# Kernel tuning notes

Hardware: AMD Instinct MI355X
Metric: run time of the kernel (lower is better)

The kernel has to match this reference:

```python
import jax, jax.numpy as jnp
import numpy as np

C_Z = 128
C_H = 128
L = 512
EPS = 1e-5


def _layer_norm(x, w, b):
    mu = jnp.mean(x, axis=-1, keepdims=True)
    var = jnp.mean(jnp.square(x - mu), axis=-1, keepdims=True)
    return (x - mu) * jax.lax.rsqrt(var + EPS) * w + b


def setup_inputs() -> dict:
    key = jax.random.key(0)
    ks = jax.random.split(key, 10)
    s_z = 1.0 / np.sqrt(C_Z)
    s_h = 1.0 / np.sqrt(C_H)
    return {
        "z": jax.random.normal(ks[0], (L, L, C_Z), dtype=jnp.float32),
        "pair_mask": jax.random.randint(ks[1], (L, L), 0, 2, dtype=jnp.int32),
        "ln_in_w": jnp.ones((C_Z,), jnp.float32),
        "ln_in_b": jnp.zeros((C_Z,), jnp.float32),
        "ln_out_w": jnp.ones((C_H,), jnp.float32),
        "ln_out_b": jnp.zeros((C_H,), jnp.float32),
        # weights stored [in, out] so forward is x @ W
        "W_proj_a": jax.random.uniform(ks[2], (C_Z, C_H), jnp.float32, -s_z, s_z),
        "W_gate_a": jax.random.uniform(ks[3], (C_Z, C_H), jnp.float32, -s_z, s_z),
        "W_proj_b": jax.random.uniform(ks[4], (C_Z, C_H), jnp.float32, -s_z, s_z),
        "W_gate_b": jax.random.uniform(ks[5], (C_Z, C_H), jnp.float32, -s_z, s_z),
        "W_gate_out": jax.random.uniform(ks[6], (C_Z, C_Z), jnp.float32, -s_z, s_z),
        "W_proj_out": jax.random.uniform(ks[7], (C_H, C_Z), jnp.float32, -s_h, s_h),
    }


def reference(z, pair_mask, ln_in_w, ln_in_b, ln_out_w, ln_out_b,
              W_proj_a, W_gate_a, W_proj_b, W_gate_b, W_gate_out, W_proj_out):
    mask = pair_mask.astype(z.dtype)[..., None]  # [L, L, 1]
    z_ln = _layer_norm(z, ln_in_w, ln_in_b)      # [L, L, c_z]
    a = jax.nn.sigmoid(z_ln @ W_gate_a) * (z_ln @ W_proj_a) * mask  # [L, L, c_h]
    b = jax.nn.sigmoid(z_ln @ W_gate_b) * (z_ln @ W_proj_b) * mask  # [L, L, c_h]
    m = jnp.einsum('ikc,jkc->ijc', a, b)         # channel-batched matmul
    m_ln = _layer_norm(m, ln_out_w, ln_out_b)
    g = jax.nn.sigmoid(z_ln @ W_gate_out)        # [L, L, c_z]
    dz = g * (m_ln @ W_proj_out)
    return dz * mask
```

## Files before the change

kernel.cpp:

```cpp
#include <hip/hip_runtime.h>
#include <stdint.h>

#define LDIM 512
#define LLTOT 262144
#define EPSV 1e-5f

typedef short bf16x8 __attribute__((ext_vector_type(8)));
typedef float f32x4 __attribute__((ext_vector_type(4)));
typedef __attribute__((address_space(1))) unsigned as1_u32;
typedef __attribute__((address_space(3))) unsigned as3_u32;

__device__ __forceinline__ void stage16(const void* g, void* l) {
  __builtin_amdgcn_global_load_lds((as1_u32*)g, (as3_u32*)l, 16, 0, 0);
}

__device__ __forceinline__ unsigned short f2bf(float f) {
  union { float f; unsigned u; } v; v.f = f;
  unsigned r = v.u + 0x7FFFu + ((v.u >> 16) & 1u);
  return (unsigned short)(r >> 16);
}
__device__ __forceinline__ float bf2f(unsigned short h) {
  union { unsigned u; float f; } v; v.u = ((unsigned)h) << 16;
  return v.f;
}
__device__ __forceinline__ unsigned cvtpk(float lo, float hi) {
  unsigned r;
  asm("v_cvt_pk_bf16_f32 %0, %1, %2" : "=v"(r) : "v"(lo), "v"(hi));
  return r;
}
__device__ __forceinline__ float exp2h(float x) {
#if __has_builtin(__builtin_amdgcn_exp2f)
  return __builtin_amdgcn_exp2f(x);
#else
  float r; asm("v_exp_f32 %0, %1" : "=v"(r) : "v"(x)); return r;
#endif
}
__device__ __forceinline__ float rcph(float x) {
#if __has_builtin(__builtin_amdgcn_rcpf)
  return __builtin_amdgcn_rcpf(x);
#else
  float r; asm("v_rcp_f32 %0, %1" : "=v"(r) : "v"(x)); return r;
#endif
}
__device__ __forceinline__ float sigm(float x) {
  return rcph(1.0f + exp2h(x * -1.44269504f));
}


__global__ void k_prep(const float* __restrict__ Wpa, const float* __restrict__ Wga,
                       const float* __restrict__ Wpb, const float* __restrict__ Wgb,
                       const float* __restrict__ Wgo, const float* __restrict__ Wpo,
                       unsigned short* __restrict__ Wt) {
  int t = blockIdx.x * blockDim.x + threadIdx.x;
  int mat = t >> 14;
  int rem = t & 16383;
  int o = rem >> 7;
  int c = rem & 127;
  const float* src;
  switch (mat) {
    case 0: src = Wga; break;
    case 1: src = Wpa; break;
    case 2: src = Wgb; break;
    case 3: src = Wpb; break;
    case 4: src = Wgo; break;
    default: src = Wpo; break;
  }
  Wt[mat * 16384 + o * 128 + c] = f2bf(src[c * 128 + o]);
}

__global__ __launch_bounds__(256, 4) void k_proj(const float* __restrict__ z,
                                                 const float* __restrict__ lnw,
                                                 const float* __restrict__ lnb,
                                                 const unsigned short* __restrict__ Wt,
                                                 const int* __restrict__ maskp,
                                                 unsigned short* __restrict__ a_f,
                                                 unsigned short* __restrict__ b_f,
                                                 unsigned short* __restrict__ gout) {
  __shared__ __align__(16) unsigned char zbuf[128 * 272];
  __shared__ float maskf[128];
  const int t = threadIdx.x;
  const int bid = blockIdx.x;
  const long r0 = (long)bid * 128;
  const int w = t >> 6, lane = t & 63;
  const int mn = lane & 15, q4 = lane >> 4;
  const int k0 = (bid & 3) * 128;
  const long ibase = (long)(bid >> 2) * 131072;

  if (t < 128) maskf[t] = (float)maskp[r0 + t];

  {
    const int sub = lane >> 4, c16 = lane & 15;
    const float4 lw0 = ((const float4*)lnw)[c16 * 2];
    const float4 lw1 = ((const float4*)lnw)[c16 * 2 + 1];
    const float4 lb0 = ((const float4*)lnb)[c16 * 2];
    const float4 lb1 = ((const float4*)lnb)[c16 * 2 + 1];
#pragma unroll 2
    for (int rr = 0; rr < 8; ++rr) {
      const int row = w * 32 + rr * 4 + sub;
      const float4* zr = (const float4*)(z + (r0 + row) * 128);
      float4 v0 = zr[c16 * 2], v1 = zr[c16 * 2 + 1];
      float s = ((v0.x + v0.y) + (v0.z + v0.w)) + ((v1.x + v1.y) + (v1.z + v1.w));
      float q = v0.x * v0.x + v0.y * v0.y + v0.z * v0.z + v0.w * v0.w +
                v1.x * v1.x + v1.y * v1.y + v1.z * v1.z + v1.w * v1.w;
#pragma unroll
      for (int off = 8; off; off >>= 1) { s += __shfl_xor(s, off); q += __shfl_xor(q, off); }
      float mu = s * (1.0f / 128.0f);
      float rs = rsqrtf(q * (1.0f / 128.0f) - mu * mu + EPSV);
      uint4 o;
      o.x = cvtpk((v0.x - mu) * rs * lw0.x + lb0.x, (v0.y - mu) * rs * lw0.y + lb0.y);
      o.y = cvtpk((v0.z - mu) * rs * lw0.z + lb0.z, (v0.w - mu) * rs * lw0.w + lb0.w);
      o.z = cvtpk((v1.x - mu) * rs * lw1.x + lb1.x, (v1.y - mu) * rs * lw1.y + lb1.y);
      o.w = cvtpk((v1.z - mu) * rs * lw1.z + lb1.z, (v1.w - mu) * rs * lw1.w + lb1.w);
      *(uint4*)(&zbuf[row * 272 + c16 * 16]) = o;
    }
  }
  __syncthreads();

#pragma unroll 1
  for (int p = 0; p < 2; ++p) {
    const unsigned short* Wg = Wt + (p * 2) * 16384;
    const unsigned short* Wp = Wt + (p * 2 + 1) * 16384;
    unsigned short* dst = p ? b_f : a_f;
    bf16x8 wg[2][4], wp[2][4];
#pragma unroll
    for (int ntl = 0; ntl < 2; ++ntl)
#pragma unroll
      for (int kk = 0; kk < 4; ++kk) {
        const int o = (w * 2 + ntl) * 16 + mn;
        wg[ntl][kk] = *(const bf16x8*)(Wg + o * 128 + kk * 32 + q4 * 8);
        wp[ntl][kk] = *(const bf16x8*)(Wp + o * 128 + kk * 32 + q4 * 8);
      }
#pragma unroll 2
    for (int rg = 0; rg < 8; ++rg) {
      bf16x8 afr[4];
#pragma unroll
      for (int kk = 0; kk < 4; ++kk)
        afr[kk] = *(const bf16x8*)(&zbuf[(rg * 16 + mn) * 272 + kk * 64 + q4 * 16]);
      f32x4 aG[2] = {{0.f,0.f,0.f,0.f},{0.f,0.f,0.f,0.f}};
      f32x4 aP[2] = {{0.f,0.f,0.f,0.f},{0.f,0.f,0.f,0.f}};
#pragma unroll
      for (int kk = 0; kk < 4; ++kk)
#pragma unroll
        for (int ntl = 0; ntl < 2; ++ntl) {
          aG[ntl] = __builtin_amdgcn_mfma_f32_16x16x32_bf16(afr[kk], wg[ntl][kk], aG[ntl], 0, 0, 0);
          aP[ntl] = __builtin_amdgcn_mfma_f32_16x16x32_bf16(afr[kk], wp[ntl][kk], aP[ntl], 0, 0, 0);
        }
      const int rowb = rg * 16 + q4 * 4;
      const int kpos = k0 + rowb;
      char* dst0 = (char*)dst + ibase + (kpos >> 5) * 8192 + (kpos & 31) * 2;
#pragma unroll
      for (int ntl = 0; ntl < 2; ++ntl) {
        const int c = (w * 2 + ntl) * 16 + mn;
        float e0 = sigm(aG[ntl][0]) * aP[ntl][0] * maskf[rowb + 0];
        float e1 = sigm(aG[ntl][1]) * aP[ntl][1] * maskf[rowb + 1];
        float e2 = sigm(aG[ntl][2]) * aP[ntl][2] * maskf[rowb + 2];
        float e3 = sigm(aG[ntl][3]) * aP[ntl][3] * maskf[rowb + 3];
        uint2 pk;
        pk.x = cvtpk(e0, e1);
        pk.y = cvtpk(e2, e3);
        *(uint2*)(dst0 + c * 64) = pk;
      }
    }
  }

  {
    const unsigned short* Wgp = Wt + 4 * 16384;
    bf16x8 wg[2][4];
#pragma unroll
    for (int ntl = 0; ntl < 2; ++ntl)
#pragma unroll
      for (int kk = 0; kk < 4; ++kk)
        wg[ntl][kk] = *(const bf16x8*)(Wgp + ((w * 2 + ntl) * 16 + mn) * 128 + kk * 32 + q4 * 8);
#pragma unroll 2
    for (int rg = 0; rg < 8; ++rg) {
      bf16x8 afr[4];
#pragma unroll
      for (int kk = 0; kk < 4; ++kk)
        afr[kk] = *(const bf16x8*)(&zbuf[(rg * 16 + mn) * 272 + kk * 64 + q4 * 16]);
      f32x4 aG[2] = {{0.f,0.f,0.f,0.f},{0.f,0.f,0.f,0.f}};
#pragma unroll
      for (int kk = 0; kk < 4; ++kk)
#pragma unroll
        for (int ntl = 0; ntl < 2; ++ntl)
          aG[ntl] = __builtin_amdgcn_mfma_f32_16x16x32_bf16(afr[kk], wg[ntl][kk], aG[ntl], 0, 0, 0);
      const int rowb = rg * 16 + q4 * 4;
#pragma unroll
      for (int ntl = 0; ntl < 2; ++ntl) {
        const int c = (w * 2 + ntl) * 16 + mn;
        unsigned u01 = cvtpk(sigm(aG[ntl][0]), sigm(aG[ntl][1]));
        unsigned u23 = cvtpk(sigm(aG[ntl][2]), sigm(aG[ntl][3]));
        gout[(r0 + rowb + 0) * 128 + c] = (unsigned short)u01;
        gout[(r0 + rowb + 1) * 128 + c] = (unsigned short)(u01 >> 16);
        gout[(r0 + rowb + 2) * 128 + c] = (unsigned short)u23;
        gout[(r0 + rowb + 3) * 128 + c] = (unsigned short)(u23 >> 16);
      }
    }
  }
}

__global__ __launch_bounds__(256, 3) void k_einsum(const unsigned short* __restrict__ af_g,
                                                   const unsigned short* __restrict__ bf_g,
                                                   unsigned short* __restrict__ m_t) {
  __shared__ __align__(16) unsigned char shm[49152];
  const int t = threadIdx.x;
  const int w = t >> 6, lane = t & 63;
  const int bid = blockIdx.x;
  const int xcd = bid & 7;
  const int j = bid >> 3;
  const int ch = xcd * 16 + (j >> 4);
  const int tile = j & 15;
  const int ti = tile >> 2, tj = tile & 3;
  const int wr = w >> 1, wc = w & 1;
  const int mn = lane & 15, q4 = lane >> 4;
  const int loff = (mn * 4 + q4) * 16;

  const long lanepart = (long)(lane >> 2) * 131072 + (lane & 3) * 16 + ch * 64;

  const char* gsrc[4];
#pragma unroll
  for (int u = 0; u < 4; ++u) {
    const int f = w * 4 + u;
    gsrc[u] = (f < 8)
        ? (const char*)af_g + (long)(ti * 8 + f) * 16 * 131072 + lanepart
        : (const char*)bf_g + (long)(tj * 8 + (f - 8)) * 16 * 131072 + lanepart;
  }

  f32x4 acc[4][4];
#pragma unroll
  for (int i = 0; i < 4; ++i)
#pragma unroll
    for (int jj = 0; jj < 4; ++jj) acc[i][jj] = (f32x4){0.f, 0.f, 0.f, 0.f};

#define STAGE(q, k32)                                                          \
  {                                                                            \
    _Pragma("unroll")                                                          \
    for (int u = 0; u < 4; ++u)                                                \
      stage16(gsrc[u] + (long)(k32) * 8192,                                    \
              &shm[(q) * 16384 + (w * 4 + u) * 1024]);                         \
  }

  STAGE(0, 0)
  STAGE(1, 1)
#pragma unroll 1
  for (int k32 = 0; k32 < 16; ++k32) {
    if (k32 < 15) {
      asm volatile("s_waitcnt vmcnt(4)\n\ts_barrier" ::: "memory");
    } else {
      asm volatile("s_waitcnt vmcnt(0)\n\ts_barrier" ::: "memory");
    }
    if (k32 + 2 < 16) STAGE((k32 + 2) % 3, k32 + 2)
    const int cb = (k32 % 3) * 16384;
    bf16x8 afr[4], bfr[4];
#pragma unroll
    for (int mt = 0; mt < 4; ++mt)
      afr[mt] = *(const bf16x8*)(&shm[cb + (wr * 4 + mt) * 1024 + loff]);
#pragma unroll
    for (int nt = 0; nt < 4; ++nt)
      bfr[nt] = *(const bf16x8*)(&shm[cb + 8192 + (wc * 4 + nt) * 1024 + loff]);
#pragma unroll
    for (int mt = 0; mt < 4; ++mt)
#pragma unroll
      for (int nt = 0; nt < 4; ++nt)
        acc[mt][nt] = __builtin_amdgcn_mfma_f32_16x16x32_bf16(
            afr[mt], bfr[nt], acc[mt][nt], 0, 0, 0);
  }
#undef STAGE
  __syncthreads();

  unsigned char* eb = shm + w * 9216;
#pragma unroll
  for (int mt = 0; mt < 4; ++mt)
#pragma unroll
    for (int nt = 0; nt < 4; ++nt) {
      const int rlb = mt * 16 + q4 * 4;
      const int cl = nt * 16 + mn;
      unsigned u01 = cvtpk(acc[mt][nt][0], acc[mt][nt][1]);
      unsigned u23 = cvtpk(acc[mt][nt][2], acc[mt][nt][3]);
      *(unsigned short*)(&eb[(rlb + 0) * 144 + cl * 2]) = (unsigned short)u01;
      *(unsigned short*)(&eb[(rlb + 1) * 144 + cl * 2]) = (unsigned short)(u01 >> 16);
      *(unsigned short*)(&eb[(rlb + 2) * 144 + cl * 2]) = (unsigned short)u23;
      *(unsigned short*)(&eb[(rlb + 3) * 144 + cl * 2]) = (unsigned short)(u23 >> 16);
    }
  char* Mg = (char*)m_t + (long)ch * 524288 +
             (long)(ti * 128 + wr * 64) * 1024 + (tj * 128 + wc * 64) * 2;
#pragma unroll
  for (int it = 0; it < 8; ++it) {
    int rl = it * 8 + (lane >> 3), cc = lane & 7;
    *(int4*)(Mg + (long)rl * 1024 + cc * 16) = *(const int4*)(&eb[rl * 144 + cc * 16]);
  }
}

__global__ __launch_bounds__(256, 4) void k_out(const unsigned short* __restrict__ m_t,
                                                const unsigned short* __restrict__ gbuf,
                                                const unsigned short* __restrict__ Wt,
                                                const int* __restrict__ maskp,
                                                const float* __restrict__ lnw,
                                                const float* __restrict__ lnb,
                                                float* __restrict__ out) {
  __shared__ unsigned char mln[64 * 272];
  __shared__ unsigned char glds[64 * 272];
  __shared__ float lw[128], lb[128], mk[64];
  const int t = threadIdx.x;
  const long r0 = (long)blockIdx.x * 64;

#pragma unroll
  for (int it = 0; it < 4; ++it) {
    int chunk = it * 256 + t;
    int c = chunk >> 3, cc = chunk & 7;
    int4 rv = *(const int4*)((const char*)m_t + (long)c * 524288 + r0 * 2 + cc * 16);
    const unsigned short* rp = (const unsigned short*)&rv;
#pragma unroll
    for (int e = 0; e < 8; ++e) {
      int er = (e + cc) & 7;
      *(unsigned short*)(&mln[(cc * 8 + er) * 272 + c * 2]) = rp[er];
    }
  }
#pragma unroll
  for (int it = 0; it < 4; ++it) {
    int chunk = it * 256 + t;
    int row = chunk >> 4, cc = chunk & 15;
    *(int4*)(&glds[row * 272 + cc * 16]) =
        *(const int4*)((const char*)gbuf + (r0 + row) * 256 + cc * 16);
  }
  if (t < 128) { lw[t] = lnw[t]; lb[t] = lnb[t]; }
  if (t < 64) mk[t] = (float)maskp[r0 + t];
  __syncthreads();

  {
    int row = t >> 2, part = t & 3;
    float xv[32];
    float s = 0.f, q = 0.f;
#pragma unroll
    for (int jj = 0; jj < 16; ++jj) {
      unsigned u = *(const unsigned*)(&mln[row * 272 + part * 64 + jj * 4]);
      float x0 = bf2f((unsigned short)(u & 0xffff));
      float x1 = bf2f((unsigned short)(u >> 16));
      xv[2 * jj] = x0; xv[2 * jj + 1] = x1;
      s += x0 + x1; q += x0 * x0 + x1 * x1;
    }
    s += __shfl_xor(s, 1); q += __shfl_xor(q, 1);
    s += __shfl_xor(s, 2); q += __shfl_xor(q, 2);
    float mu = s * (1.f / 128.f);
    float var = q * (1.f / 128.f) - mu * mu;
    float rs = rsqrtf(var + EPSV);
#pragma unroll
    for (int jj = 0; jj < 16; ++jj) {
      int c = part * 32 + 2 * jj;
      unsigned pk = cvtpk((xv[2 * jj] - mu) * rs * lw[c] + lb[c],
                          (xv[2 * jj + 1] - mu) * rs * lw[c + 1] + lb[c + 1]);
      *(unsigned*)(&mln[row * 272 + c * 2]) = pk;
    }
  }
  __syncthreads();

  const int w = t >> 6, lane = t & 63;
  const int mn = lane & 15, q4 = lane >> 4;
  bf16x8 afr[4];
#pragma unroll
  for (int kk = 0; kk < 4; ++kk)
    afr[kk] = *(const bf16x8*)(&mln[(w * 16 + mn) * 272 + kk * 64 + q4 * 16]);
  const unsigned short* Wp = Wt + 5 * 16384;
#pragma unroll 1
  for (int nt = 0; nt < 8; ++nt) {
    f32x4 acc = {0.f, 0.f, 0.f, 0.f};
#pragma unroll
    for (int kk = 0; kk < 4; ++kk) {
      bf16x8 bfr = *(const bf16x8*)(Wp + (nt * 16 + mn) * 128 + kk * 32 + q4 * 8);
      acc = __builtin_amdgcn_mfma_f32_16x16x32_bf16(afr[kk], bfr, acc, 0, 0, 0);
    }
    const int cl = nt * 16 + mn;
#pragma unroll
    for (int r = 0; r < 4; ++r) {
      const int row = w * 16 + q4 * 4 + r;
      float gv = bf2f(*(const unsigned short*)(&glds[row * 272 + cl * 2]));
      out[(r0 + row) * 128 + cl] = acc[r] * gv * mk[row];
    }
  }
}

extern "C" void kernel_launch(void* const* d_in, const int* in_sizes, int n_in,
                              void* d_out, int out_size, void* d_ws, size_t ws_size,
                              hipStream_t stream) {
  const float* z    = (const float*)d_in[0];
  const int* maskp  = (const int*)d_in[1];
  const float* lniw = (const float*)d_in[2];
  const float* lnib = (const float*)d_in[3];
  const float* lnow = (const float*)d_in[4];
  const float* lnob = (const float*)d_in[5];
  const float* Wpa  = (const float*)d_in[6];
  const float* Wga  = (const float*)d_in[7];
  const float* Wpb  = (const float*)d_in[8];
  const float* Wgb  = (const float*)d_in[9];
  const float* Wgo  = (const float*)d_in[10];
  const float* Wpo  = (const float*)d_in[11];
  float* out = (float*)d_out;

  char* ws = (char*)d_ws;
  unsigned short* a_f = (unsigned short*)(ws);
  unsigned short* b_f = (unsigned short*)(ws + 67108864);
  unsigned short* g   = (unsigned short*)(ws + 134217728);
  unsigned short* m_t = (unsigned short*)(ws + 201326592);
  unsigned short* Wt  = (unsigned short*)(ws + 268435456);

  k_prep<<<384, 256, 0, stream>>>(Wpa, Wga, Wpb, Wgb, Wgo, Wpo, Wt);
  k_proj<<<2048, 256, 0, stream>>>(z, lniw, lnib, Wt, maskp, a_f, b_f, g);
  k_einsum<<<2048, 256, 0, stream>>>(a_f, b_f, m_t);
  k_out<<<4096, 256, 0, stream>>>(m_t, g, Wt, maskp, lnow, lnob, out);
}
```

Measured before the change: 485.3 us.

## Enlarge einsum tiles to 256x256 with 512-thread blocks and double buffering

The channel-batched einsum kernel now computes a 256x256 output tile per block using 8 waves, each holding an 8x4 grid of MFMA accumulators, instead of 128x128 tiles with 4 waves. This cuts global reads of the a/b operands per output element. The three-stage async LDS pipeline becomes a two-buffer scheme that waits for all loads and syncs at the end of every k-step, so less load latency is hidden. The epilogue is split into four passes through a smaller per-wave LDS scratch. The larger accumulator set raises register pressure and limits occupancy to two blocks.

```diff
diff --git a/kernel.cpp b/kernel.cpp
--- a/kernel.cpp
+++ b/kernel.cpp
@@ -198,19 +198,19 @@
   }
 }
 
-__global__ __launch_bounds__(256, 3) void k_einsum(const unsigned short* __restrict__ af_g,
+__global__ __launch_bounds__(512, 2) void k_einsum(const unsigned short* __restrict__ af_g,
                                                    const unsigned short* __restrict__ bf_g,
                                                    unsigned short* __restrict__ m_t) {
-  __shared__ __align__(16) unsigned char shm[49152];
+  __shared__ __align__(16) unsigned char shm[65536];
   const int t = threadIdx.x;
   const int w = t >> 6, lane = t & 63;
   const int bid = blockIdx.x;
   const int xcd = bid & 7;
   const int j = bid >> 3;
-  const int ch = xcd * 16 + (j >> 4);
-  const int tile = j & 15;
-  const int ti = tile >> 2, tj = tile & 3;
-  const int wr = w >> 1, wc = w & 1;
+  const int ch = xcd * 16 + (j >> 2);
+  const int tile = j & 3;
+  const int ti = tile >> 1, tj = tile & 1;
+  const int wr = w >> 2, wc = w & 3;
   const int mn = lane & 15, q4 = lane >> 4;
   const int loff = (mn * 4 + q4) * 16;
 
@@ -220,14 +220,14 @@
 #pragma unroll
   for (int u = 0; u < 4; ++u) {
     const int f = w * 4 + u;
-    gsrc[u] = (f < 8)
-        ? (const char*)af_g + (long)(ti * 8 + f) * 16 * 131072 + lanepart
-        : (const char*)bf_g + (long)(tj * 8 + (f - 8)) * 16 * 131072 + lanepart;
-  }
-
-  f32x4 acc[4][4];
-#pragma unroll
-  for (int i = 0; i < 4; ++i)
+    gsrc[u] = (f < 16)
+        ? (const char*)af_g + (long)(ti * 256 + f * 16) * 131072 + lanepart
+        : (const char*)bf_g + (long)(tj * 256 + (f - 16) * 16) * 131072 + lanepart;
+  }
+
+  f32x4 acc[8][4];
+#pragma unroll
+  for (int i = 0; i < 8; ++i)
 #pragma unroll
     for (int jj = 0; jj < 4; ++jj) acc[i][jj] = (f32x4){0.f, 0.f, 0.f, 0.f};
 
@@ -236,57 +236,62 @@
     _Pragma("unroll")                                                          \
     for (int u = 0; u < 4; ++u)                                                \
       stage16(gsrc[u] + (long)(k32) * 8192,                                    \
-              &shm[(q) * 16384 + (w * 4 + u) * 1024]);                         \
-  }
-
+              &shm[(q) * 32768 + (w * 4 + u) * 1024]);                         \
+  }
+
+  int cur = 0;
   STAGE(0, 0)
-  STAGE(1, 1)
+  asm volatile("s_waitcnt vmcnt(0)" ::: "memory");
+  __syncthreads();
 #pragma unroll 1
   for (int k32 = 0; k32 < 16; ++k32) {
-    if (k32 < 15) {
-      asm volatile("s_waitcnt vmcnt(4)\n\ts_barrier" ::: "memory");
-    } else {
-      asm volatile("s_waitcnt vmcnt(0)\n\ts_barrier" ::: "memory");
-    }
-    if (k32 + 2 < 16) STAGE((k32 + 2) % 3, k32 + 2)
-    const int cb = (k32 % 3) * 16384;
-    bf16x8 afr[4], bfr[4];
-#pragma unroll
-    for (int mt = 0; mt < 4; ++mt)
-      afr[mt] = *(const bf16x8*)(&shm[cb + (wr * 4 + mt) * 1024 + loff]);
+    if (k32 < 15) STAGE(cur ^ 1, k32 + 1)
+    const int cb = cur * 32768;
+    bf16x8 afr[8], bfr[4];
+#pragma unroll
+    for (int mt = 0; mt < 8; ++mt)
+      afr[mt] = *(const bf16x8*)(&shm[cb + (wr * 8 + mt) * 1024 + loff]);
 #pragma unroll
     for (int nt = 0; nt < 4; ++nt)
-      bfr[nt] = *(const bf16x8*)(&shm[cb + 8192 + (wc * 4 + nt) * 1024 + loff]);
-#pragma unroll
-    for (int mt = 0; mt < 4; ++mt)
+      bfr[nt] = *(const bf16x8*)(&shm[cb + 16384 + (wc * 4 + nt) * 1024 + loff]);
+#pragma unroll
+    for (int mt = 0; mt < 8; ++mt)
 #pragma unroll
       for (int nt = 0; nt < 4; ++nt)
         acc[mt][nt] = __builtin_amdgcn_mfma_f32_16x16x32_bf16(
             afr[mt], bfr[nt], acc[mt][nt], 0, 0, 0);
+    asm volatile("s_waitcnt vmcnt(0)" ::: "memory");
+    __syncthreads();
+    cur ^= 1;
   }
 #undef STAGE
-  __syncthreads();
-
-  unsigned char* eb = shm + w * 9216;
-#pragma unroll
-  for (int mt = 0; mt < 4; ++mt)
-#pragma unroll
-    for (int nt = 0; nt < 4; ++nt) {
-      const int rlb = mt * 16 + q4 * 4;
-      const int cl = nt * 16 + mn;
-      unsigned u01 = cvtpk(acc[mt][nt][0], acc[mt][nt][1]);
-      unsigned u23 = cvtpk(acc[mt][nt][2], acc[mt][nt][3]);
-      *(unsigned short*)(&eb[(rlb + 0) * 144 + cl * 2]) = (unsigned short)u01;
-      *(unsigned short*)(&eb[(rlb + 1) * 144 + cl * 2]) = (unsigned short)(u01 >> 16);
-      *(unsigned short*)(&eb[(rlb + 2) * 144 + cl * 2]) = (unsigned short)u23;
-      *(unsigned short*)(&eb[(rlb + 3) * 144 + cl * 2]) = (unsigned short)(u23 >> 16);
-    }
-  char* Mg = (char*)m_t + (long)ch * 524288 +
-             (long)(ti * 128 + wr * 64) * 1024 + (tj * 128 + wc * 64) * 2;
-#pragma unroll
-  for (int it = 0; it < 8; ++it) {
-    int rl = it * 8 + (lane >> 3), cc = lane & 7;
-    *(int4*)(Mg + (long)rl * 1024 + cc * 16) = *(const int4*)(&eb[rl * 144 + cc * 16]);
+
+  unsigned char* eb = shm + w * 4352;
+  const long mgbase = (long)ch * 524288 +
+                      (long)(ti * 256 + wr * 128) * 1024 + (tj * 256 + wc * 64) * 2;
+#pragma unroll 1
+  for (int p = 0; p < 4; ++p) {
+#pragma unroll
+    for (int mtl = 0; mtl < 2; ++mtl)
+#pragma unroll
+      for (int nt = 0; nt < 4; ++nt) {
+        const int rlb = mtl * 16 + q4 * 4;
+        const int cl = nt * 16 + mn;
+        const f32x4 a4 = acc[p * 2 + mtl][nt];
+        unsigned u01 = cvtpk(a4[0], a4[1]);
+        unsigned u23 = cvtpk(a4[2], a4[3]);
+        *(unsigned short*)(&eb[(rlb + 0) * 136 + cl * 2]) = (unsigned short)u01;
+        *(unsigned short*)(&eb[(rlb + 1) * 136 + cl * 2]) = (unsigned short)(u01 >> 16);
+        *(unsigned short*)(&eb[(rlb + 2) * 136 + cl * 2]) = (unsigned short)u23;
+        *(unsigned short*)(&eb[(rlb + 3) * 136 + cl * 2]) = (unsigned short)(u23 >> 16);
+      }
+#pragma unroll
+    for (int it2 = 0; it2 < 4; ++it2) {
+      const int idx = it2 * 64 + lane;
+      const int rl = idx >> 3, cc = idx & 7;
+      *(int4*)((char*)m_t + mgbase + (long)(p * 32 + rl) * 1024 + cc * 16) =
+          *(const int4*)(&eb[rl * 136 + cc * 16]);
+    }
   }
 }
 
@@ -404,6 +409,6 @@
 
   k_prep<<<384, 256, 0, stream>>>(Wpa, Wga, Wpb, Wgb, Wgo, Wpo, Wt);
   k_proj<<<2048, 256, 0, stream>>>(z, lniw, lnib, Wt, maskp, a_f, b_f, g);
-  k_einsum<<<2048, 256, 0, stream>>>(a_f, b_f, m_t);
+  k_einsum<<<512, 512, 0, stream>>>(a_f, b_f, m_t);
   k_out<<<4096, 256, 0, stream>>>(m_t, g, Wt, maskp, lnow, lnob, out);
 }
```

New measurement: 843.4 us. 73.8% more time.
